# Performance work log

Measured on AMD Instinct MI355X. Metric: run time of the kernel, lower is better.

The kernel has to match this reference:

```python
import jax, jax.numpy as jnp
import numpy as np

KSIZE = 5
PAD = 2  # replicate padding per side for 'same' 5x5x5 box filter


def setup_inputs() -> dict:
    key = jax.random.key(0)
    # mp: [N, C, D, H, W] nonnegative probability maps
    mp = jax.random.uniform(key, (1, 21, 16, 256, 256), dtype=jnp.float32)
    return {"mp": mp}


def reference(mp):
    N, C, D, H, W = mp.shape
    # replicate ('edge') padding on D, H, W, then depthwise 5x5x5 box filter
    x = jnp.pad(mp, ((0, 0), (0, 0), (PAD, PAD), (PAD, PAD), (PAD, PAD)), mode="edge")
    k = jnp.full((C, 1, KSIZE, KSIZE, KSIZE), 1.0 / (KSIZE ** 3), dtype=mp.dtype)
    y = jax.lax.conv_general_dilated(
        x, k,
        window_strides=(1, 1, 1),
        padding="VALID",
        dimension_numbers=("NCDHW", "OIDHW", "NCDHW"),
        feature_group_count=C,
    )  # [N, C, D, H, W]

    # normalize over channel axis (torch permutes to put channels first; we keep axis=1)
    y = y / jnp.sum(y, axis=1, keepdims=True)

    # weighted-median selection: running cumulative sum over channels
    s = jnp.cumsum(y, axis=1)                     # [N, C, D, H, W]
    idx = jnp.arange(C).reshape(1, C, 1, 1, 1)    # channel indices

    # med0: LAST channel i with y[i] > 0 and cumsum < 0.5 (torch loop overwrites), default 0
    med0 = jnp.maximum(
        jnp.max(jnp.where((y > 0) & (s < 0.5), idx, -1), axis=1, keepdims=True), 0
    )
    # med1: torch sets med[1] only while med[1]==0, so the result is the FIRST
    # NONZERO channel with cumsum > 0.5 (i=0 qualifying leaves med[1]==0 and gets
    # overwritten by the next qualifying i); 0 if no nonzero channel qualifies.
    med1 = jnp.argmax((s > 0.5) & (idx > 0), axis=1, keepdims=True)

    keep = (idx == med0) | (idx == med1)
    return jnp.where(keep, y, jnp.zeros((), dtype=y.dtype))
```

## Files before the change

### kernel.cpp

```cpp
#include <hip/hip_runtime.h>

#define CC   21
#define DD   16
#define HH   256
#define WW   256
#define HWP  (HH * WW)
#define DHW  (DD * HWP)

typedef float f4a __attribute__((ext_vector_type(4), aligned(16)));
__device__ __forceinline__ f4a f4add(f4a a, f4a b) { return a + b; }

#define AROW 36
#define PYN  12
#define A_SZ (DD * PYN * AROW)

#define NB1  (8 * 32 * CC)
#define CHK1 (NB1 / 8)

__global__ __launch_bounds__(256, 5) void dh_blur_kernel(const float* __restrict__ mp,
                                                         float* __restrict__ out) {
    __shared__ float A[A_SZ];
    const int tid = threadIdx.x;

    const int bid = blockIdx.x;
    const int t   = (bid & 7) * CHK1 + (bid >> 3);
    const int yb  = t & 31;
    const int wt  = (t >> 5) & 7;
    const int ch  = t >> 8;
    const int w0  = wt * 32;
    const int h0  = yb * 8;

    if (tid < 96) {
        const int py = tid >> 3;
        const int x4 = tid & 7;
        const int h  = min(HH - 1, max(0, h0 + py - 2));
        const float* colp = mp + (size_t)ch * DHW + (size_t)h * WW + w0 + x4 * 4;

        f4a P[16];
#pragma unroll
        for (int d = 0; d < 16; ++d) P[d] = *(const f4a*)(colp + (size_t)d * HWP);

        constexpr int M0[12] = {0, 0, 0, 1, 2, 3, 4, 5, 6, 7, 8, 9};
        constexpr int M1[12] = {6, 7, 8, 9, 10, 11, 12, 13, 14, 15, 15, 15};

        {
            f4a sum = f4add(f4add(f4add(P[M0[0]], P[M0[1]]),
                                  f4add(P[M0[2]], P[M0[3]])), P[M0[4]]);
#pragma unroll
            for (int i = 0; i < 8; ++i) {
                *(f4a*)(&A[(i * PYN + py) * AROW + x4 * 4]) = sum;
                if (i < 7) sum = sum - P[M0[i]] + P[M0[i + 5]];
            }
        }
        {
            f4a sum = f4add(f4add(f4add(P[M1[0]], P[M1[1]]),
                                  f4add(P[M1[2]], P[M1[3]])), P[M1[4]]);
#pragma unroll
            for (int i = 0; i < 8; ++i) {
                *(f4a*)(&A[((8 + i) * PYN + py) * AROW + x4 * 4]) = sum;
                if (i < 7) sum = sum - P[M1[i]] + P[M1[i + 5]];
            }
        }
    }
    __syncthreads();

#pragma unroll
    for (int it = 0; it < 4; ++it) {
        const int tt   = tid + it * 256;
        const int xx4  = tt & 7;
        const int y    = (tt >> 3) & 7;
        const int dout = tt >> 6;

        const float* b = &A[(dout * PYN + y) * AROW + xx4 * 4];
        f4a a = *(const f4a*)b;
#pragma unroll
        for (int k = 1; k < 5; ++k) a = f4add(a, *(const f4a*)(b + k * AROW));

        *(f4a*)(out + (size_t)ch * DHW + (size_t)dout * HWP
                + (h0 + y) * WW + w0 + xx4 * 4) = a;
    }
}

#define ROWP 264

__global__ __launch_bounds__(256) void wmedian_kernel(float* __restrict__ y4) {
    __shared__ float R[CC * ROWP];

    const int h = blockIdx.x;
    const int d = blockIdx.y;
    const int tid = threadIdx.x;
    float* __restrict__ base = y4 + (size_t)d * HWP + (size_t)h * WW;

    for (int idx = tid; idx < CC * 64; idx += 256) {
        const int c  = idx >> 6;
        const int w4 = idx & 63;
        *(f4a*)(&R[c * ROWP + 4 + w4 * 4]) = *(const f4a*)(base + (size_t)c * DHW + w4 * 4);
    }
    if (tid < CC) {
        const float v0 = base[(size_t)tid * DHW];
        const float vL = base[(size_t)tid * DHW + (WW - 1)];
        R[tid * ROWP + 2]   = v0;
        R[tid * ROWP + 3]   = v0;
        R[tid * ROWP + 260] = vL;
        R[tid * ROWP + 261] = vL;
    }
    __syncthreads();

    const int w = tid;
    float v[CC];
    float tot = 0.f;
#pragma unroll
    for (int c = 0; c < CC; ++c) {
        const float* r = &R[c * ROWP + 2 + w];
        v[c] = ((((r[0] + r[1]) + r[2]) + r[3]) + r[4]);
        tot += v[c];
    }
    const float inv = 1.0f / tot;

    float s = 0.f, sv0 = 0.f, sv1 = 0.f;
    int m0 = 0, m1 = 0;
#pragma unroll
    for (int c = 0; c < CC; ++c) {
        const float yn = v[c] * inv;
        const float sn = s + yn;
        if (c == 0) { sv0 = yn; sv1 = yn; }
        if (v[c] > 0.f && sn < 0.5f) { m0 = c; sv0 = yn; }
        if (m1 == 0 && c > 0 && sn > 0.5f) { m1 = c; sv1 = yn; }
        s = sn;
    }

#pragma unroll
    for (int c = 0; c < CC; ++c) {
        base[(size_t)c * DHW + w] = (c == m0) ? sv0 : ((c == m1) ? sv1 : 0.f);
    }
}

extern "C" void kernel_launch(void* const* d_in, const int* in_sizes, int n_in,
                              void* d_out, int out_size, void* d_ws, size_t ws_size,
                              hipStream_t stream) {
    const float* mp = (const float*)d_in[0];
    float* out = (float*)d_out;

    dh_blur_kernel<<<NB1, 256, 0, stream>>>(mp, out);
    wmedian_kernel<<<dim3(HH, DD), 256, 0, stream>>>(out);
}
```

Before: 185.8 us.

## Process 32-row H segments per block with a ring buffer to reuse halo rows

Each blur block now covers 32 output rows instead of 8 and keeps the D-blurred rows in a 16-row circular shared buffer. Only 8 new input rows are staged per 8-row step, so the 4-row H halo is no longer re-read and re-blurred for every 8-row tile. The cost is four times fewer blocks, extra __syncthreads between steps, and staging that runs on only 64 threads in series with the output work. Occupancy hint lowered to 4 to match the larger shared buffer.

```diff
diff --git a/kernel.cpp b/kernel.cpp
--- a/kernel.cpp
+++ b/kernel.cpp
@@ -11,73 +11,87 @@
 __device__ __forceinline__ f4a f4add(f4a a, f4a b) { return a + b; }
 
 #define AROW 36
-#define PYN  12
-#define A_SZ (DD * PYN * AROW)
+#define PYR  16
+#define A_SZ (DD * PYR * AROW)
 
-#define NB1  (8 * 32 * CC)
+#define NSEG 8
+#define NB1  (8 * NSEG * CC)
 #define CHK1 (NB1 / 8)
 
-__global__ __launch_bounds__(256, 5) void dh_blur_kernel(const float* __restrict__ mp,
+__device__ __forceinline__ void stage_col(const float* __restrict__ src, int h0seg,
+                                          int idx, int x4, float* __restrict__ A) {
+    const int h = min(HH - 1, max(0, h0seg + idx - 2));
+    const float* colp = src + (size_t)h * WW + x4 * 4;
+    const int phys = idx & 15;
+
+    f4a P[16];
+#pragma unroll
+    for (int d = 0; d < 16; ++d) P[d] = *(const f4a*)(colp + (size_t)d * HWP);
+
+    constexpr int M0[12] = {0, 0, 0, 1, 2, 3, 4, 5, 6, 7, 8, 9};
+    constexpr int M1[12] = {6, 7, 8, 9, 10, 11, 12, 13, 14, 15, 15, 15};
+
+    {
+        f4a sum = f4add(f4add(f4add(P[M0[0]], P[M0[1]]),
+                              f4add(P[M0[2]], P[M0[3]])), P[M0[4]]);
+#pragma unroll
+        for (int i = 0; i < 8; ++i) {
+            *(f4a*)(&A[(i * PYR + phys) * AROW + x4 * 4]) = sum;
+            if (i < 7) sum = sum - P[M0[i]] + P[M0[i + 5]];
+        }
+    }
+    {
+        f4a sum = f4add(f4add(f4add(P[M1[0]], P[M1[1]]),
+                              f4add(P[M1[2]], P[M1[3]])), P[M1[4]]);
+#pragma unroll
+        for (int i = 0; i < 8; ++i) {
+            *(f4a*)(&A[((8 + i) * PYR + phys) * AROW + x4 * 4]) = sum;
+            if (i < 7) sum = sum - P[M1[i]] + P[M1[i + 5]];
+        }
+    }
+}
+
+__global__ __launch_bounds__(256, 4) void dh_blur_kernel(const float* __restrict__ mp,
                                                          float* __restrict__ out) {
     __shared__ float A[A_SZ];
     const int tid = threadIdx.x;
 
-    const int bid = blockIdx.x;
-    const int t   = (bid & 7) * CHK1 + (bid >> 3);
-    const int yb  = t & 31;
-    const int wt  = (t >> 5) & 7;
-    const int ch  = t >> 8;
-    const int w0  = wt * 32;
-    const int h0  = yb * 8;
+    const int bid  = blockIdx.x;
+    const int t    = (bid & 7) * CHK1 + (bid >> 3);
+    const int wt   = t & 7;
+    const int hseg = (t >> 3) & 7;
+    const int ch   = t >> 6;
+    const int w0   = wt * 32;
+    const int h0seg = hseg * 32;
+    const float* __restrict__ src = mp + (size_t)ch * DHW + w0;
 
-    if (tid < 96) {
-        const int py = tid >> 3;
-        const int x4 = tid & 7;
-        const int h  = min(HH - 1, max(0, h0 + py - 2));
-        const float* colp = mp + (size_t)ch * DHW + (size_t)h * WW + w0 + x4 * 4;
-
-        f4a P[16];
-#pragma unroll
-        for (int d = 0; d < 16; ++d) P[d] = *(const f4a*)(colp + (size_t)d * HWP);
-
-        constexpr int M0[12] = {0, 0, 0, 1, 2, 3, 4, 5, 6, 7, 8, 9};
-        constexpr int M1[12] = {6, 7, 8, 9, 10, 11, 12, 13, 14, 15, 15, 15};
-
-        {
-            f4a sum = f4add(f4add(f4add(P[M0[0]], P[M0[1]]),
-                                  f4add(P[M0[2]], P[M0[3]])), P[M0[4]]);
-#pragma unroll
-            for (int i = 0; i < 8; ++i) {
-                *(f4a*)(&A[(i * PYN + py) * AROW + x4 * 4]) = sum;
-                if (i < 7) sum = sum - P[M0[i]] + P[M0[i + 5]];
-            }
-        }
-        {
-            f4a sum = f4add(f4add(f4add(P[M1[0]], P[M1[1]]),
-                                  f4add(P[M1[2]], P[M1[3]])), P[M1[4]]);
-#pragma unroll
-            for (int i = 0; i < 8; ++i) {
-                *(f4a*)(&A[((8 + i) * PYN + py) * AROW + x4 * 4]) = sum;
-                if (i < 7) sum = sum - P[M1[i]] + P[M1[i + 5]];
-            }
-        }
-    }
+    if (tid < 96) stage_col(src, h0seg, tid >> 3, tid & 7, A);
     __syncthreads();
 
 #pragma unroll
-    for (int it = 0; it < 4; ++it) {
-        const int tt   = tid + it * 256;
-        const int xx4  = tt & 7;
-        const int y    = (tt >> 3) & 7;
-        const int dout = tt >> 6;
+    for (int k = 0; k < 4; ++k) {
+#pragma unroll
+        for (int it = 0; it < 4; ++it) {
+            const int tt   = tid + it * 256;
+            const int xx4  = tt & 7;
+            const int y    = (tt >> 3) & 7;
+            const int dout = tt >> 6;
+            const int idx0 = 8 * k + y;
 
-        const float* b = &A[(dout * PYN + y) * AROW + xx4 * 4];
-        f4a a = *(const f4a*)b;
+            f4a a = *(const f4a*)(&A[(dout * PYR + (idx0 & 15)) * AROW + xx4 * 4]);
 #pragma unroll
-        for (int k = 1; k < 5; ++k) a = f4add(a, *(const f4a*)(b + k * AROW));
+            for (int kk = 1; kk < 5; ++kk)
+                a = f4add(a, *(const f4a*)(&A[(dout * PYR + ((idx0 + kk) & 15)) * AROW + xx4 * 4]));
 
-        *(f4a*)(out + (size_t)ch * DHW + (size_t)dout * HWP
-                + (h0 + y) * WW + w0 + xx4 * 4) = a;
+            *(f4a*)(out + (size_t)ch * DHW + (size_t)dout * HWP
+                    + (size_t)(h0seg + 8 * k + y) * WW + w0 + xx4 * 4) = a;
+        }
+
+        if (k < 3) {
+            __syncthreads();
+            if (tid < 64) stage_col(src, h0seg, 8 * (k + 1) + 4 + (tid >> 3), tid & 7, A);
+            __syncthreads();
+        }
     }
 }
 
```

Result: slower. 192.7 us (+3.7%).

## Stage blur input tile into LDS with direct global-to-LDS loads

Applied to the files above, without the earlier changes.

The first blur kernel no longer has 96 threads each load sixteen depth slices from global memory into registers. All 256 threads now issue 16-byte global_load_lds transfers that place the padded input tile straight into shared memory, and the D-axis sliding sum then reads and writes that buffer in place. The LDS layout drops the 36-float row padding for a dense 32-float stride, which matches the DMA lane order. The aim is more memory-level parallelism and fewer idle threads during the load phase. The cost is an extra barrier and reliance on correct vmcnt waits before LDS reads, plus possible bank conflicts from the unpadded stride.

```diff
diff --git a/kernel.cpp b/kernel.cpp
--- a/kernel.cpp
+++ b/kernel.cpp
@@ -10,16 +10,20 @@
 typedef float f4a __attribute__((ext_vector_type(4), aligned(16)));
 __device__ __forceinline__ f4a f4add(f4a a, f4a b) { return a + b; }
 
-#define AROW 36
-#define PYN  12
-#define A_SZ (DD * PYN * AROW)
+#define GLDS16(gp, lp)                                                        \
+    __builtin_amdgcn_global_load_lds(                                         \
+        (const __attribute__((address_space(1))) void*)(gp),                  \
+        (__attribute__((address_space(3))) void*)(lp), 16, 0, 0)
+
+#define A_SZ (DD * PYN_ * 32)
+#define PYN_ 12
 
 #define NB1  (8 * 32 * CC)
 #define CHK1 (NB1 / 8)
 
 __global__ __launch_bounds__(256, 5) void dh_blur_kernel(const float* __restrict__ mp,
                                                          float* __restrict__ out) {
-    __shared__ float A[A_SZ];
+    __shared__ float A[DD * PYN_ * 32];
     const int tid = threadIdx.x;
 
     const int bid = blockIdx.x;
@@ -29,16 +33,34 @@
     const int ch  = t >> 8;
     const int w0  = wt * 32;
     const int h0  = yb * 8;
+    const float* __restrict__ src = mp + (size_t)ch * DHW + w0;
+
+    {
+        const int wv   = tid >> 6;
+        const int lane = tid & 63;
+#pragma unroll
+        for (int j = 0; j < 6; ++j) {
+            const int inst = wv * 6 + j;
+            const int idx4 = inst * 64 + lane;
+            const int d    = idx4 / 96;
+            const int r    = idx4 - d * 96;
+            const int py   = r >> 3;
+            const int x4   = r & 7;
+            const int h    = min(HH - 1, max(0, h0 + py - 2));
+            const float* gp = src + (size_t)d * HWP + (size_t)h * WW + x4 * 4;
+            GLDS16(gp, &A[inst * 256]);
+        }
+    }
+    __syncthreads();
 
     if (tid < 96) {
         const int py = tid >> 3;
         const int x4 = tid & 7;
-        const int h  = min(HH - 1, max(0, h0 + py - 2));
-        const float* colp = mp + (size_t)ch * DHW + (size_t)h * WW + w0 + x4 * 4;
+        float* colA = &A[py * 32 + x4 * 4];
 
         f4a P[16];
 #pragma unroll
-        for (int d = 0; d < 16; ++d) P[d] = *(const f4a*)(colp + (size_t)d * HWP);
+        for (int d = 0; d < 16; ++d) P[d] = *(const f4a*)(colA + d * 384);
 
         constexpr int M0[12] = {0, 0, 0, 1, 2, 3, 4, 5, 6, 7, 8, 9};
         constexpr int M1[12] = {6, 7, 8, 9, 10, 11, 12, 13, 14, 15, 15, 15};
@@ -48,7 +70,7 @@
                                   f4add(P[M0[2]], P[M0[3]])), P[M0[4]]);
 #pragma unroll
             for (int i = 0; i < 8; ++i) {
-                *(f4a*)(&A[(i * PYN + py) * AROW + x4 * 4]) = sum;
+                *(f4a*)(colA + i * 384) = sum;
                 if (i < 7) sum = sum - P[M0[i]] + P[M0[i + 5]];
             }
         }
@@ -57,7 +79,7 @@
                                   f4add(P[M1[2]], P[M1[3]])), P[M1[4]]);
 #pragma unroll
             for (int i = 0; i < 8; ++i) {
-                *(f4a*)(&A[((8 + i) * PYN + py) * AROW + x4 * 4]) = sum;
+                *(f4a*)(colA + (8 + i) * 384) = sum;
                 if (i < 7) sum = sum - P[M1[i]] + P[M1[i + 5]];
             }
         }
@@ -71,13 +93,13 @@
         const int y    = (tt >> 3) & 7;
         const int dout = tt >> 6;
 
-        const float* b = &A[(dout * PYN + y) * AROW + xx4 * 4];
+        const float* b = &A[dout * 384 + y * 32 + xx4 * 4];
         f4a a = *(const f4a*)b;
 #pragma unroll
-        for (int k = 1; k < 5; ++k) a = f4add(a, *(const f4a*)(b + k * AROW));
+        for (int k = 1; k < 5; ++k) a = f4add(a, *(const f4a*)(b + k * 32));
 
         *(f4a*)(out + (size_t)ch * DHW + (size_t)dout * HWP
-                + (h0 + y) * WW + w0 + xx4 * 4) = a;
+                + (size_t)(h0 + y) * WW + w0 + xx4 * 4) = a;
     }
 }
 
```

New measurement: 185.4 us. Within noise of the previous version (-0.2%).
